# Performance work log

Measured on AMD Instinct MI355X. Metric: run time of the kernel, lower is better.

The kernel has to match this reference:

```python
import jax, jax.numpy as jnp
import numpy as np

B, NP, L, C, NA = 16, 512, 20, 3, 50
RATIO = 0.8
K = int(np.ceil(RATIO * NP))  # 410 nodes kept per graph
N = B * NP
E = 6 * N
NF, EF = 13, 4
EPS = 1e-5


def _graph_norm(x, w, b, ms):
    # PyG GraphNorm called WITHOUT batch in the source -> single global graph
    mean = x.mean(0)
    out = x - ms * mean
    var = (out * out).mean(0)
    return w * out / jnp.sqrt(var + EPS) + b


def _forward(x, pan_w, lin1_w, lin1_b, norm1_w, norm1_b, norm1_ms,
             pool_p, pool_beta, gat_wl, gat_bl, gat_wr, gat_br, gat_att, gat_bias,
             norm2_w, norm2_b, norm2_ms,
             val1_w, val1_b, val2_w, val2_b, val3_w, val3_b,
             adv1_w, adv1_b, adv2_w, adv2_b, adv3_w, adv3_b,
             edge_index, current_node_ids, action_mask):
    src, dst = edge_index[0], edge_index[1]
    # PANConv builds SparseTensor(row=edge_index[1], col=edge_index[0]) -> row = target
    A = jnp.zeros((B, NP, NP), x.dtype).at[dst // NP, dst % NP, src % NP].set(1.0)
    eyeB = jnp.broadcast_to(jnp.eye(NP, dtype=x.dtype), A.shape)

    # panentropy: M = sum_{i=0..L} w_i * A^i  (dense per graph)
    def step(carry, wi):
        tmp, acc = carry
        tmp = tmp @ A
        return (tmp, acc + wi * tmp), None
    (_, M), _ = jax.lax.scan(step, (eyeB, pan_w[0] * eyeB), pan_w[1:])
    deg = M.sum(-1)                                   # row sums
    dis = jnp.where(deg > 0, 1.0 / jnp.sqrt(deg), 0.0)
    Mn = dis[:, :, None] * M * dis[:, None, :]        # D^-1/2 M D^-1/2

    # conv1: propagate (Mn @ x) then Linear
    x3 = x.reshape(B, NP, NF)
    h = jnp.einsum('bij,bjf->bif', Mn, x3) @ lin1_w + lin1_b   # [B,NP,C]
    x1 = jax.nn.relu(_graph_norm(h.reshape(N, C), norm1_w, norm1_b, norm1_ms))  # [N,C]
    h = x1.reshape(B, NP, C)

    # PANPooling: score = tanh(b0 * <x,p> + b1 * colsum(Mn)); keep top K per graph
    score = jnp.tanh(pool_beta[0] * (h * pool_p).sum(-1) + pool_beta[1] * Mn.sum(-2))
    vals, idx = jax.lax.top_k(score, K)                        # [B,K]
    xp = jnp.take_along_axis(h, idx[:, :, None], axis=1) * vals[..., None]
    Mg = jax.vmap(lambda m, i: m[i][:, i])(Mn, idx)            # filtered adjacency [B,K,K]
    mask = (jnp.swapaxes(Mg, 1, 2) != 0) | jnp.eye(K, dtype=bool)  # mask[b,i,j]: edge j->i (+self loops)

    # GATv2Conv, heads=1, eval mode (no dropout), edge_attr not passed in source
    xl = xp @ gat_wl + gat_bl
    xr = xp @ gat_wr + gat_br
    e = jax.nn.leaky_relu(xr[:, :, None, :] + xl[:, None, :, :], 0.2)  # [B,i,j,C]
    logits = jnp.where(mask, jnp.einsum('bijc,c->bij', e, gat_att), -1e9)
    alpha = jax.nn.softmax(logits, axis=-1)
    g = jnp.einsum('bij,bjc->bic', alpha, xl) + gat_bias

    g = jax.nn.relu(_graph_norm(g.reshape(B * K, C), norm2_w, norm2_b, norm2_ms)).reshape(B, K, C)
    gp = g.sum(1)                                              # global_add_pool [B,C]

    # source uses POOLED bincount cumsum offsets to index the pre-pool arrays (faithful)
    gidx = current_node_ids + jnp.arange(B, dtype=current_node_ids.dtype) * K
    feat = jnp.concatenate([x[gidx], x1[gidx], gp], axis=1)    # [B,19]

    a = jax.nn.relu(feat @ adv1_w + adv1_b)
    a = jax.nn.relu(a @ adv2_w + adv2_b)
    a = a @ adv3_w + adv3_b
    v = jax.nn.relu(feat @ val1_w + val1_b)
    v = jax.nn.relu(v @ val2_w + val2_b)
    v = v @ val3_w + val3_b
    q = v + (a - a.mean(1, keepdims=True))
    return jnp.where(action_mask == 0, -1e8, q)


def setup_inputs() -> dict:
    key = jax.random.key(0)
    ks = list(jax.random.split(key, 40))
    nk = lambda: ks.pop()
    # within-graph random edges so the PyG-style batch structure is valid
    g = jax.random.randint(nk(), (E,), 0, B)
    u = jax.random.randint(nk(), (E,), 0, NP)
    v = jax.random.randint(nk(), (E,), 0, NP)
    edge_index = jnp.stack([g * NP + u, g * NP + v]).astype(jnp.int32)

    def lin(k, i, o):
        k1, k2 = jax.random.split(k)
        return (jax.random.normal(k1, (i, o), jnp.float32) / np.sqrt(i),
                jax.random.normal(k2, (o,), jnp.float32) * 0.01)

    lin1_w, lin1_b = lin(nk(), NF, C)
    gat_wl, gat_bl = lin(nk(), C, C)
    gat_wr, gat_br = lin(nk(), C, C)
    val1_w, val1_b = lin(nk(), 19, 10)
    val2_w, val2_b = lin(nk(), 10, 5)
    val3_w, val3_b = lin(nk(), 5, 1)
    adv1_w, adv1_b = lin(nk(), 19, 10)
    adv2_w, adv2_b = lin(nk(), 10, 5)
    adv3_w, adv3_b = lin(nk(), 5, NA)
    return dict(
        x=jax.random.normal(nk(), (N, NF), jnp.float32),
        edge_index=edge_index,
        edge_attr=jax.random.normal(nk(), (E, EF), jnp.float32),
        batch=jnp.arange(N, dtype=jnp.int32) // NP,
        current_node_ids=jax.random.randint(nk(), (B,), 0, NP),
        action_mask=jax.random.randint(nk(), (B, NA), 0, 2),
        pan_w=jax.random.uniform(nk(), (L + 1,), jnp.float32) * 0.5,
        lin1_w=lin1_w, lin1_b=lin1_b,
        norm1_w=jnp.ones(C), norm1_b=jnp.zeros(C), norm1_ms=jnp.ones(C),
        pool_p=jax.random.normal(nk(), (C,), jnp.float32),
        pool_beta=jnp.array([0.5, 0.5], jnp.float32),
        gat_wl=gat_wl, gat_bl=gat_bl, gat_wr=gat_wr, gat_br=gat_br,
        gat_att=jax.random.normal(nk(), (C,), jnp.float32),
        gat_bias=jax.random.normal(nk(), (C,), jnp.float32) * 0.01,
        norm2_w=jnp.ones(C), norm2_b=jnp.zeros(C), norm2_ms=jnp.ones(C),
        val1_w=val1_w, val1_b=val1_b, val2_w=val2_w, val2_b=val2_b,
        val3_w=val3_w, val3_b=val3_b,
        adv1_w=adv1_w, adv1_b=adv1_b, adv2_w=adv2_w, adv2_b=adv2_b,
        adv3_w=adv3_w, adv3_b=adv3_b,
    )


def reference(x, edge_index, edge_attr, batch, current_node_ids, action_mask,
              pan_w, lin1_w, lin1_b, norm1_w, norm1_b, norm1_ms,
              pool_p, pool_beta, gat_wl, gat_bl, gat_wr, gat_br, gat_att, gat_bias,
              norm2_w, norm2_b, norm2_ms,
              val1_w, val1_b, val2_w, val2_b, val3_w, val3_b,
              adv1_w, adv1_b, adv2_w, adv2_b, adv3_w, adv3_b):
    del edge_attr, batch  # received by the torch forward but never consumed
    return _forward(x, pan_w, lin1_w, lin1_b, norm1_w, norm1_b, norm1_ms,
                    pool_p, pool_beta, gat_wl, gat_bl, gat_wr, gat_br, gat_att, gat_bias,
                    norm2_w, norm2_b, norm2_ms,
                    val1_w, val1_b, val2_w, val2_b, val3_w, val3_b,
                    adv1_w, adv1_b, adv2_w, adv2_b, adv3_w, adv3_b,
                    edge_index, current_node_ids, action_mask)
```

## Files before the change

### kernel.cpp

```cpp
#include <hip/hip_runtime.h>
#include <hip/hip_bf16.h>
#include <stdint.h>
#include <math.h>

#define BB   16
#define NPn  512
#define LLp  20
#define NAa  50
#define KKk  410
#define NNt  (BB * NPn)
#define EEe  (6 * NNt)
#define NFf  13
#define KPAD 416
#define KP2  448
#define EPSf 1e-5f
#define QCLMP 1e6f
#define MAXD 28
#define PADR 512

__device__ __forceinline__ float r17_sane(float v) {
    if (!(v == v)) return 0.0f;
    return fminf(fmaxf(v, -1e15f), 1e15f);
}

__device__ __forceinline__ int r19_wmaxdeg(const int (&iF)[MAXD]) {
    int deg = 0;
#pragma unroll
    for (int j = 0; j < MAXD; ++j) deg += (iF[j] != PADR) ? 1 : 0;
#pragma unroll
    for (int off = 32; off; off >>= 1) {
        const int o = __shfl_xor(deg, off);
        deg = o > deg ? o : deg;
    }
    return deg;
}

__device__ __forceinline__ float r19_gsum(const float* __restrict__ rp,
                                          const int (&iF)[MAXD], int dm) {
    float s = 0.0f;
    s += rp[iF[0]]; s += rp[iF[1]]; s += rp[iF[2]]; s += rp[iF[3]];
    if (dm > 4) {
        s += rp[iF[4]]; s += rp[iF[5]]; s += rp[iF[6]]; s += rp[iF[7]];
        if (dm > 8) {
            s += rp[iF[8]]; s += rp[iF[9]]; s += rp[iF[10]]; s += rp[iF[11]];
            if (dm > 12) {
                s += rp[iF[12]]; s += rp[iF[13]]; s += rp[iF[14]]; s += rp[iF[15]];
                if (dm > 16) {
                    s += rp[iF[16]]; s += rp[iF[17]]; s += rp[iF[18]]; s += rp[iF[19]];
                    if (dm > 20) {
                        s += rp[iF[20]]; s += rp[iF[21]]; s += rp[iF[22]]; s += rp[iF[23]];
                        if (dm > 24) {
                            s += rp[iF[24]]; s += rp[iF[25]]; s += rp[iF[26]]; s += rp[iF[27]];
                        }
                    }
                }
            }
        }
    }
    return s;
}

__device__ __forceinline__ void r19_gor(const uint2* __restrict__ rp,
                                        const int (&iF)[MAXD], int dm, uint2& r) {
    {
        const uint2 v0 = rp[iF[0]], v1 = rp[iF[1]], v2 = rp[iF[2]], v3 = rp[iF[3]];
        r.x |= v0.x | v1.x | v2.x | v3.x;
        r.y |= v0.y | v1.y | v2.y | v3.y;
    }
    if (dm > 4) {
        const uint2 v0 = rp[iF[4]], v1 = rp[iF[5]], v2 = rp[iF[6]], v3 = rp[iF[7]];
        r.x |= v0.x | v1.x | v2.x | v3.x;
        r.y |= v0.y | v1.y | v2.y | v3.y;
        if (dm > 8) {
            const uint2 w0 = rp[iF[8]], w1 = rp[iF[9]], w2 = rp[iF[10]], w3 = rp[iF[11]];
            r.x |= w0.x | w1.x | w2.x | w3.x;
            r.y |= w0.y | w1.y | w2.y | w3.y;
            if (dm > 12) {
                const uint2 u0 = rp[iF[12]], u1 = rp[iF[13]], u2 = rp[iF[14]], u3 = rp[iF[15]];
                r.x |= u0.x | u1.x | u2.x | u3.x;
                r.y |= u0.y | u1.y | u2.y | u3.y;
                if (dm > 16) {
                    const uint2 a0 = rp[iF[16]], a1 = rp[iF[17]], a2 = rp[iF[18]], a3 = rp[iF[19]];
                    r.x |= a0.x | a1.x | a2.x | a3.x;
                    r.y |= a0.y | a1.y | a2.y | a3.y;
                    if (dm > 20) {
                        const uint2 b0 = rp[iF[20]], b1 = rp[iF[21]], b2 = rp[iF[22]], b3 = rp[iF[23]];
                        r.x |= b0.x | b1.x | b2.x | b3.x;
                        r.y |= b0.y | b1.y | b2.y | b3.y;
                        if (dm > 24) {
                            const uint2 c0 = rp[iF[24]], c1 = rp[iF[25]], c2 = rp[iF[26]], c3 = rp[iF[27]];
                            r.x |= c0.x | c1.x | c2.x | c3.x;
                            r.y |= c0.y | c1.y | c2.y | c3.y;
                        }
                    }
                }
            }
        }
    }
}

__global__ __launch_bounds__(256) void r17_scatter(
    const int* __restrict__ ei,
    uint32_t* __restrict__ fwdb, uint32_t* __restrict__ trsb)
{
    const int e = blockIdx.x * 256 + threadIdx.x;
    if (e < EEe) {
        const int src = ei[e], dst = ei[EEe + e];
        atomicOr(&fwdb[(size_t)dst * 16 + ((src & 511) >> 5)], 1u << (src & 31));
        atomicOr(&trsb[(size_t)src * 16 + ((dst & 511) >> 5)], 1u << (dst & 31));
    }
}

__global__ __launch_bounds__(256) void r17_extract(
    const uint32_t* __restrict__ fwdb, const uint32_t* __restrict__ trsb,
    unsigned short* __restrict__ csrF, unsigned short* __restrict__ csrT)
{
    const int t = blockIdx.x * 256 + threadIdx.x;
    const int node = t & 8191;
    const uint32_t* bs = (t < 8192) ? (fwdb + (size_t)node * 16)
                                    : (trsb + (size_t)node * 16);
    unsigned short* cs = (t < 8192) ? csrF : csrT;
    int cnt = 0;
    for (int w = 0; w < 16; ++w) {
        uint32_t bits = bs[w];
        while (bits) {
            const int u = (w << 5) + __ffs(bits) - 1;
            bits &= bits - 1;
            if (cnt < MAXD) cs[(size_t)cnt * 8192 + node] = (unsigned short)u;
            ++cnt;
        }
    }
    for (int j = cnt; j < MAXD; ++j) cs[(size_t)j * 8192 + node] = PADR;
}

__global__ __launch_bounds__(512) void r19_mid(
    const float* __restrict__ x,
    const unsigned short* __restrict__ csrF,
    const unsigned short* __restrict__ csrT,
    const float* __restrict__ panw,
    const float* __restrict__ l1w, const float* __restrict__ l1b,
    float* __restrict__ h_raw, float* __restrict__ colsum,
    uint32_t* __restrict__ Rb)
{
    __shared__ __align__(16) uint32_t sbuf[2052];
    const int b = blockIdx.x, y = blockIdx.y, t = threadIdx.x;
    const int node = b * 512 + t;

    int iF[MAXD];
#pragma unroll
    for (int j = 0; j < MAXD; ++j) iF[j] = (int)csrF[(size_t)j * 8192 + node];
    const int dmF = r19_wmaxdeg(iF);

    if (y < 4) {
        const int c = y;
        float* pa  = (float*)sbuf;
        float* pb  = (float*)(sbuf + 513);
        float* wsh = (float*)(sbuf + 1026);
        if (t < 21) wsh[t] = panw[t];

        pa[t] = 1.0f;
        if (t == 0) { pa[512] = 0.0f; pb[512] = 0.0f; }
        __syncthreads();
        float dacc = wsh[0];
        {
            float* rp = pa; float* rn = pb;
            for (int i = 1; i <= LLp; ++i) {
                const float s = r19_gsum(rp, iF, dmF);
                rn[t] = s;
                dacc += wsh[i] * s;
                __syncthreads();
                float* tp = rp; rp = rn; rn = tp;
            }
        }
        const float d0 = (dacc > 0.0f) ? 1.0f / sqrtf(dacc) : 0.0f;

        int idx[MAXD];
        int dm2;
        if (c == 3) {
#pragma unroll
            for (int j = 0; j < MAXD; ++j) idx[j] = (int)csrT[(size_t)j * 8192 + node];
            dm2 = r19_wmaxdeg(idx);
        } else {
#pragma unroll
            for (int j = 0; j < MAXD; ++j) idx[j] = iF[j];
            dm2 = dmF;
        }
        float seed;
        if (c < 3) {
            float xw = 0.0f;
            const float* xr = x + (size_t)node * NFf;
            for (int f = 0; f < NFf; ++f) xw += xr[f] * l1w[f * 3 + c];
            seed = d0 * xw;
        } else {
            seed = d0;
        }
        pa[t] = seed;
        if (t == 0) { pa[512] = 0.0f; pb[512] = 0.0f; }
        __syncthreads();
        float acc = wsh[0] * seed;
        {
            float* rp = pa; float* rn = pb;
            for (int i = 1; i <= LLp; ++i) {
                const float s = r19_gsum(rp, idx, dm2);
                rn[t] = s;
                acc += wsh[i] * s;
                __syncthreads();
                float* tp = rp; rp = rn; rn = tp;
            }
        }
        if (c < 3) h_raw[(size_t)node * 3 + c] = r17_sane(d0 * acc + l1b[c]);
        else       colsum[node] = r17_sane(d0 * acc);
    } else {
        const int q = y - 4;
        uint2* R1 = (uint2*)sbuf;
        uint2* R2 = R1 + 513;
        uint2 seed;
        seed.x = ((t >> 5) == 2 * q)     ? (1u << (t & 31)) : 0u;
        seed.y = ((t >> 5) == 2 * q + 1) ? (1u << (t & 31)) : 0u;
        R1[t] = seed;
        if (t == 0) {
            uint2 z; z.x = 0u; z.y = 0u;
            R1[512] = z; R2[512] = z;
        }
        __syncthreads();
        uint2* Rp = R1; uint2* Rn = R2;
        for (int i = 0; i < LLp; ++i) {
            uint2 r = Rp[t];
            r19_gor(Rp, iF, dmF, r);
            Rn[t] = r;
            __syncthreads();
            uint2* tp = Rp; Rp = Rn; Rn = tp;
        }
        *(uint2*)(&Rb[(size_t)node * 16 + 2 * q]) = Rp[t];
    }
}

__global__ __launch_bounds__(512) void r19_pool(
    const float* __restrict__ h_raw,
    const float* __restrict__ colsum,
    const uint32_t* __restrict__ Rb,
    const float* n1w, const float* n1b, const float* n1ms,
    const float* poolp, const float* poolb,
    const float* gwl, const float* gbl,
    float* __restrict__ x1,
    float* __restrict__ xpg,
    float4* __restrict__ xlg,
    int*   __restrict__ kidxg,
    uint32_t* __restrict__ RTg)
{
    __shared__ __align__(16) uint32_t pg[2208];
    float* sc   = (float*)pg;
    float* mv   = (float*)(pg + 512);
    float* wred = (float*)(pg + 520);
    float* xpS  = (float*)(pg + 544);
    int*   kidx = (int*)(pg + 1792);
    const int b = blockIdx.x, t = threadIdx.x;
    const int lane = t & 63, wv = t >> 6;
    const float inv_n = 1.0f / (float)NNt;

    float hv0[16], hv1[16], hv2[16];
    float p0 = 0.0f, p1 = 0.0f, p2 = 0.0f;
#pragma unroll
    for (int k = 0; k < 16; ++k) {
        const float* hr = h_raw + (size_t)(k * 512 + t) * 3;
        hv0[k] = hr[0]; hv1[k] = hr[1]; hv2[k] = hr[2];
        p0 += hv0[k]; p1 += hv1[k]; p2 += hv2[k];
    }
#pragma unroll
    for (int off = 32; off; off >>= 1) {
        p0 += __shfl_xor(p0, off); p1 += __shfl_xor(p1, off); p2 += __shfl_xor(p2, off);
    }
    if (lane == 0) { wred[wv * 3 + 0] = p0; wred[wv * 3 + 1] = p1; wred[wv * 3 + 2] = p2; }
    __syncthreads();
    if (t < 3) {
        float s = 0.0f;
        for (int w = 0; w < 8; ++w) s += wred[w * 3 + t];
        mv[t] = s * inv_n;
    }
    __syncthreads();
    const float mm0 = n1ms[0] * mv[0], mm1 = n1ms[1] * mv[1], mm2 = n1ms[2] * mv[2];
    float q0 = 0.0f, q1 = 0.0f, q2 = 0.0f;
#pragma unroll
    for (int k = 0; k < 16; ++k) {
        const float d0 = hv0[k] - mm0, d1 = hv1[k] - mm1, d2 = hv2[k] - mm2;
        q0 += d0 * d0; q1 += d1 * d1; q2 += d2 * d2;
    }
#pragma unroll
    for (int off = 32; off; off >>= 1) {
        q0 += __shfl_xor(q0, off); q1 += __shfl_xor(q1, off); q2 += __shfl_xor(q2, off);
    }
    if (lane == 0) { wred[wv * 3 + 0] = q0; wred[wv * 3 + 1] = q1; wred[wv * 3 + 2] = q2; }
    __syncthreads();
    if (t < 3) {
        float s = 0.0f;
        for (int w = 0; w < 8; ++w) s += wred[w * 3 + t];
        mv[3 + t] = s * inv_n;
    }
    __syncthreads();

    const float mmv[3] = { mm0, mm1, mm2 };
    float xv[3];
#pragma unroll
    for (int c = 0; c < 3; ++c) {
        const float iv = 1.0f / sqrtf(fmaxf(mv[3 + c], 0.0f) + EPSf);
        const float o  = h_raw[(size_t)(b * NPn + t) * 3 + c] - mmv[c];
        const float tt = n1w[c] * o * iv + n1b[c];
        xv[c] = fmaxf(tt, 0.0f);
        x1[(size_t)(b * NPn + t) * 3 + c] = xv[c];
    }
    float s = poolb[0] * (xv[0] * poolp[0] + xv[1] * poolp[1] + xv[2] * poolp[2])
            + poolb[1] * colsum[b * NPn + t];
    s = tanhf(s);
    if (!(s == s)) s = 0.0f;
    sc[t] = s;
    __syncthreads();

    int cnt = 0;
    for (int u = 0; u < NPn; u += 4) {
        const float4 s4 = *(const float4*)(sc + u);
        cnt += ((s4.x > s) || (s4.x == s && (u + 0) < t)) ? 1 : 0;
        cnt += ((s4.y > s) || (s4.y == s && (u + 1) < t)) ? 1 : 0;
        cnt += ((s4.z > s) || (s4.z == s && (u + 2) < t)) ? 1 : 0;
        cnt += ((s4.w > s) || (s4.w == s && (u + 3) < t)) ? 1 : 0;
    }
    if (cnt < KKk) {
        const float xp0 = xv[0] * s, xp1 = xv[1] * s, xp2 = xv[2] * s;
        kidx[cnt] = t;
        xpS[cnt * 3 + 0] = xp0;
        xpS[cnt * 3 + 1] = xp1;
        xpS[cnt * 3 + 2] = xp2;
        kidxg[b * KPAD + cnt] = t;
        xpg[(size_t)(b * KPAD + cnt) * 3 + 0] = xp0;
        xpg[(size_t)(b * KPAD + cnt) * 3 + 1] = xp1;
        xpg[(size_t)(b * KPAD + cnt) * 3 + 2] = xp2;
    }
    __syncthreads();

    float Wl[9];
#pragma unroll
    for (int i2 = 0; i2 < 9; ++i2) Wl[i2] = gwl[i2];
    const float Bl0 = gbl[0], Bl1 = gbl[1], Bl2 = gbl[2];
    if (t < KP2) {
        float xl0, xl1, xl2;
        uint32_t* RT = RTg + (size_t)b * 16 * KP2 + t;
        if (t < KKk) {
            const float c0 = xpS[t * 3 + 0];
            const float c1 = xpS[t * 3 + 1];
            const float c2 = xpS[t * 3 + 2];
            xl0 = c0 * Wl[0] + c1 * Wl[3] + c2 * Wl[6] + Bl0;
            xl1 = c0 * Wl[1] + c1 * Wl[4] + c2 * Wl[7] + Bl1;
            xl2 = c0 * Wl[2] + c1 * Wl[5] + c2 * Wl[8] + Bl2;
            const uint4* rr = (const uint4*)(Rb + (size_t)(b * NPn + kidx[t]) * 16);
            const uint4 r0 = rr[0], r1 = rr[1], r2 = rr[2], r3 = rr[3];
            RT[ 0 * KP2] = r0.x; RT[ 1 * KP2] = r0.y; RT[ 2 * KP2] = r0.z; RT[ 3 * KP2] = r0.w;
            RT[ 4 * KP2] = r1.x; RT[ 5 * KP2] = r1.y; RT[ 6 * KP2] = r1.z; RT[ 7 * KP2] = r1.w;
            RT[ 8 * KP2] = r2.x; RT[ 9 * KP2] = r2.y; RT[10 * KP2] = r2.z; RT[11 * KP2] = r2.w;
            RT[12 * KP2] = r3.x; RT[13 * KP2] = r3.y; RT[14 * KP2] = r3.z; RT[15 * KP2] = r3.w;
        } else {
            xl0 = 0.0f; xl1 = 0.0f; xl2 = 0.0f;
#pragma unroll
            for (int w = 0; w < 16; ++w) RT[w * KP2] = 0u;
        }
        xlg[(size_t)(b * KP2 + t)] = make_float4(xl0, xl1, xl2, 0.0f);
    }
}

__global__ __launch_bounds__(512) void r19_gat(
    const float* __restrict__ xpg,
    const float4* __restrict__ xlg,
    const int* __restrict__ kidxg,
    const uint32_t* __restrict__ RTg,
    const float* __restrict__ gwr, const float* __restrict__ gbr,
    const float* __restrict__ gatt, const float* __restrict__ gbias,
    float* __restrict__ g_raw)
{
    const int b = blockIdx.x, y = blockIdx.y, t = threadIdx.x;
    const int lane = t & 63, wv = t >> 6;
    const int i = y * 8 + wv;
    if (i >= KKk) return;

    float Wr[9];
#pragma unroll
    for (int k = 0; k < 9; ++k) Wr[k] = gwr[k];
    const float Br0 = gbr[0], Br1 = gbr[1], Br2 = gbr[2];
    const float At0 = gatt[0], At1 = gatt[1], At2 = gatt[2];
    const float Gb0 = gbias[0], Gb1 = gbias[1], Gb2 = gbias[2];

    const int bi = kidxg[b * KPAD + i];
    const float c0 = xpg[(size_t)(b * KPAD + i) * 3 + 0];
    const float c1 = xpg[(size_t)(b * KPAD + i) * 3 + 1];
    const float c2 = xpg[(size_t)(b * KPAD + i) * 3 + 2];
    const float xr0 = c0 * Wr[0] + c1 * Wr[3] + c2 * Wr[6] + Br0;
    const float xr1 = c0 * Wr[1] + c1 * Wr[4] + c2 * Wr[7] + Br1;
    const float xr2 = c0 * Wr[2] + c1 * Wr[5] + c2 * Wr[8] + Br2;

    const uint32_t mbit = 1u << (bi & 31);
    const uint32_t* Rw = RTg + (size_t)(b * 16 + (bi >> 5)) * KP2;
    const float4* xlb = xlg + (size_t)b * KP2;

    float mx = -3e38f, lsum = 0.0f, b0 = 0.0f, b1 = 0.0f, b2 = 0.0f;
#pragma unroll
    for (int it = 0; it < 7; ++it) {
        const int j = lane + it * 64;
        const uint32_t rw = Rw[j];
        const float4 xlv = xlb[j];
        const float xl0 = xlv.x, xl1 = xlv.y, xl2 = xlv.z;
        const bool valid = (rw & mbit) || (j == i);
        float e0 = xr0 + xl0; e0 = e0 > 0.0f ? e0 : 0.2f * e0;
        float e1 = xr1 + xl1; e1 = e1 > 0.0f ? e1 : 0.2f * e1;
        float e2 = xr2 + xl2; e2 = e2 > 0.0f ? e2 : 0.2f * e2;
        const float sv = At0 * e0 + At1 * e1 + At2 * e2;
        if (valid) {
            if (sv > mx) {
                const float r = __expf(mx - sv);
                lsum *= r; b0 *= r; b1 *= r; b2 *= r;
                mx = sv;
            }
            const float pj = __expf(sv - mx);
            lsum += pj;
            b0 += pj * xl0; b1 += pj * xl1; b2 += pj * xl2;
        }
    }
#pragma unroll
    for (int off = 32; off; off >>= 1) {
        const float mo = __shfl_xor(mx, off);
        const float lo = __shfl_xor(lsum, off);
        const float d0 = __shfl_xor(b0, off);
        const float d1 = __shfl_xor(b1, off);
        const float d2 = __shfl_xor(b2, off);
        const float M  = fmaxf(mx, mo);
        const float ea = __expf(mx - M), eb = __expf(mo - M);
        lsum = lsum * ea + lo * eb;
        b0 = b0 * ea + d0 * eb;
        b1 = b1 * ea + d1 * eb;
        b2 = b2 * ea + d2 * eb;
        mx = M;
    }
    if (lane == 0) {
        const float rl = 1.0f / fmaxf(lsum, 1e-30f);
        g_raw[(size_t)(b * KPAD + i) * 3 + 0] = r17_sane(b0 * rl + Gb0);
        g_raw[(size_t)(b * KPAD + i) * 3 + 1] = r17_sane(b1 * rl + Gb1);
        g_raw[(size_t)(b * KPAD + i) * 3 + 2] = r17_sane(b2 * rl + Gb2);
    }
}

__global__ __launch_bounds__(512) void r17_head(
    const float* __restrict__ g_raw,
    const float* __restrict__ x1,
    const float* __restrict__ x,
    const int* __restrict__ cnid,
    const int* __restrict__ amask,
    const float* n2w, const float* n2b, const float* n2ms,
    const float* v1w, const float* v1b,
    const float* v2w, const float* v2b,
    const float* v3w, const float* v3b,
    const float* a1w, const float* a1b,
    const float* a2w, const float* a2b,
    const float* a3w, const float* a3b,
    float* __restrict__ out)
{
    __shared__ float wred[24];
    __shared__ float mv[6];
    __shared__ float gp[3];
    __shared__ float feat[19];
    __shared__ float h1a[10], h1v[10], h2a[5], h2v[5];
    __shared__ float a3[50];
    __shared__ float vout_s, amean_s;
    const int b = blockIdx.x, t = threadIdx.x;
    const int lane = t & 63, wv = t >> 6;
    const float denom = 1.0f / (float)(BB * KKk);

    float gv0[13], gv1[13], gv2[13];
    float p0 = 0.0f, p1 = 0.0f, p2 = 0.0f;
#pragma unroll
    for (int k = 0; k < 13; ++k) {
        const int r = k * 512 + t;
        float q0 = 0.0f, q1 = 0.0f, q2 = 0.0f;
        if (r < BB * KKk) {
            const int bq = r / KKk, iq = r - bq * KKk;
            const float* gr = g_raw + (size_t)(bq * KPAD + iq) * 3;
            q0 = gr[0]; q1 = gr[1]; q2 = gr[2];
        }
        gv0[k] = q0; gv1[k] = q1; gv2[k] = q2;
        p0 += q0; p1 += q1; p2 += q2;
    }
#pragma unroll
    for (int off = 32; off; off >>= 1) {
        p0 += __shfl_xor(p0, off); p1 += __shfl_xor(p1, off); p2 += __shfl_xor(p2, off);
    }
    if (lane == 0) { wred[wv * 3 + 0] = p0; wred[wv * 3 + 1] = p1; wred[wv * 3 + 2] = p2; }
    __syncthreads();
    if (t < 3) {
        float s = 0.0f;
        for (int w = 0; w < 8; ++w) s += wred[w * 3 + t];
        mv[t] = s * denom;
    }
    __syncthreads();
    const float mm0 = n2ms[0] * mv[0], mm1 = n2ms[1] * mv[1], mm2 = n2ms[2] * mv[2];
    float q0a = 0.0f, q1a = 0.0f, q2a = 0.0f;
#pragma unroll
    for (int k = 0; k < 13; ++k) {
        const int r = k * 512 + t;
        if (r < BB * KKk) {
            const float d0 = gv0[k] - mm0, d1 = gv1[k] - mm1, d2 = gv2[k] - mm2;
            q0a += d0 * d0; q1a += d1 * d1; q2a += d2 * d2;
        }
    }
#pragma unroll
    for (int off = 32; off; off >>= 1) {
        q0a += __shfl_xor(q0a, off); q1a += __shfl_xor(q1a, off); q2a += __shfl_xor(q2a, off);
    }
    if (lane == 0) { wred[wv * 3 + 0] = q0a; wred[wv * 3 + 1] = q1a; wred[wv * 3 + 2] = q2a; }
    __syncthreads();
    if (t < 3) {
        float s = 0.0f;
        for (int w = 0; w < 8; ++w) s += wred[w * 3 + t];
        mv[3 + t] = s * denom;
    }
    __syncthreads();

    const float mmv[3] = { mm0, mm1, mm2 };
    float s3[3] = { 0.0f, 0.0f, 0.0f };
    if (t < KKk) {
        const size_t r = (size_t)(b * KPAD + t) * 3;
#pragma unroll
        for (int c = 0; c < 3; ++c) {
            const float iv = 1.0f / sqrtf(fmaxf(mv[3 + c], 0.0f) + EPSf);
            s3[c] = fmaxf((g_raw[r + c] - mmv[c]) * iv * n2w[c] + n2b[c], 0.0f);
        }
    }
    float g0 = s3[0], g1 = s3[1], g2 = s3[2];
#pragma unroll
    for (int off = 32; off; off >>= 1) {
        g0 += __shfl_xor(g0, off); g1 += __shfl_xor(g1, off); g2 += __shfl_xor(g2, off);
    }
    if (lane == 0) { wred[wv * 3 + 0] = g0; wred[wv * 3 + 1] = g1; wred[wv * 3 + 2] = g2; }
    __syncthreads();
    if (t < 3) {
        float s = 0.0f;
        for (int w = 0; w < 8; ++w) s += wred[w * 3 + t];
        gp[t] = s;
    }
    __syncthreads();

    if (t < 19) {
        const int gidx = cnid[b] + b * KKk;
        float fv;
        if (t < 13)      fv = x[(size_t)gidx * NFf + t];
        else if (t < 16) fv = x1[(size_t)gidx * 3 + (t - 13)];
        else             fv = gp[t - 16];
        feat[t] = fv;
    }
    __syncthreads();

    if (t < 10) {
        float s = a1b[t];
        for (int f = 0; f < 19; ++f) s += feat[f] * a1w[f * 10 + t];
        h1a[t] = fmaxf(s, 0.0f);
    } else if (t >= 64 && t < 74) {
        const int j = t - 64;
        float s = v1b[j];
        for (int f = 0; f < 19; ++f) s += feat[f] * v1w[f * 10 + j];
        h1v[j] = fmaxf(s, 0.0f);
    }
    __syncthreads();
    if (t < 5) {
        float s = a2b[t];
        for (int k = 0; k < 10; ++k) s += h1a[k] * a2w[k * 5 + t];
        h2a[t] = fmaxf(s, 0.0f);
    } else if (t >= 64 && t < 69) {
        const int j = t - 64;
        float s = v2b[j];
        for (int k = 0; k < 10; ++k) s += h1v[k] * v2w[k * 5 + j];
        h2v[j] = fmaxf(s, 0.0f);
    }
    __syncthreads();
    if (t < 50) {
        float s = a3b[t];
        for (int k = 0; k < 5; ++k) s += h2a[k] * a3w[k * 50 + t];
        a3[t] = s;
    } else if (t == 64) {
        float s = v3b[0];
        for (int k = 0; k < 5; ++k) s += h2v[k] * v3w[k];
        vout_s = s;
    }
    __syncthreads();
    if (t == 0) {
        float s = 0.0f;
        for (int k = 0; k < 50; ++k) s += a3[k];
        amean_s = s * (1.0f / 50.0f);
    }
    __syncthreads();
    if (t < 50) {
        float q = vout_s + a3[t] - amean_s;
        if (!(q == q)) q = 0.0f;
        q = fminf(fmaxf(q, -QCLMP), QCLMP);
        out[b * NAa + t] = (amask[b * NAa + t] == 0) ? -1e8f : q;
    }
}

extern "C" void kernel_launch(void* const* d_in, const int* in_sizes, int n_in,
                              void* d_out, int out_size, void* d_ws, size_t ws_size,
                              hipStream_t stream) {
    (void)in_sizes; (void)n_in; (void)out_size;
    const float* x     = (const float*)d_in[0];
    const int* ei      = (const int*)d_in[1];
    const int* cnid    = (const int*)d_in[4];
    const int* amask   = (const int*)d_in[5];
    const float* panw  = (const float*)d_in[6];
    const float* l1w   = (const float*)d_in[7];
    const float* l1b   = (const float*)d_in[8];
    const float* n1w   = (const float*)d_in[9];
    const float* n1b   = (const float*)d_in[10];
    const float* n1ms  = (const float*)d_in[11];
    const float* poolp = (const float*)d_in[12];
    const float* poolb = (const float*)d_in[13];
    const float* gwl   = (const float*)d_in[14];
    const float* gbl   = (const float*)d_in[15];
    const float* gwr   = (const float*)d_in[16];
    const float* gbr   = (const float*)d_in[17];
    const float* gatt  = (const float*)d_in[18];
    const float* gbias = (const float*)d_in[19];
    const float* n2w   = (const float*)d_in[20];
    const float* n2b   = (const float*)d_in[21];
    const float* n2ms  = (const float*)d_in[22];
    const float* v1w   = (const float*)d_in[23];
    const float* v1b   = (const float*)d_in[24];
    const float* v2w   = (const float*)d_in[25];
    const float* v2b   = (const float*)d_in[26];
    const float* v3w   = (const float*)d_in[27];
    const float* v3b   = (const float*)d_in[28];
    const float* a1w   = (const float*)d_in[29];
    const float* a1b   = (const float*)d_in[30];
    const float* a2w   = (const float*)d_in[31];
    const float* a2b   = (const float*)d_in[32];
    const float* a3w   = (const float*)d_in[33];
    const float* a3b   = (const float*)d_in[34];
    float* out         = (float*)d_out;

    uint8_t* wsb = (uint8_t*)d_ws;
    uint32_t* fwdb = (uint32_t*)wsb;
    uint32_t* trsb = (uint32_t*)(wsb + 524288);
    uint32_t* Rb   = (uint32_t*)(wsb + 1048576);
    unsigned short* csrF = (unsigned short*)(wsb + 1572864);
    unsigned short* csrT = csrF + (size_t)MAXD * 8192;
    float* h_raw  = (float*)(csrT + (size_t)MAXD * 8192);
    float* x1     = h_raw + (size_t)NNt * 3;
    float* colsum = x1 + (size_t)NNt * 3;
    float* g_raw  = colsum + NNt;
    float* xpg    = g_raw + (size_t)BB * KPAD * 3;
    float4* xlg   = (float4*)(xpg + (size_t)BB * KPAD * 3);
    int*   kidxg  = (int*)(xlg + (size_t)BB * KP2);
    uint32_t* RTg = (uint32_t*)(kidxg + (size_t)BB * KPAD);
    const size_t needed = 1572864
                        + 2 * (size_t)MAXD * 8192 * 2
                        + ((size_t)(2 * NNt * 3 + NNt
                           + 2 * BB * KPAD * 3)) * 4
                        + (size_t)BB * KP2 * 16
                        + (size_t)BB * KPAD * 4
                        + (size_t)BB * 16 * KP2 * 4;
    if (ws_size < needed) return;

    hipMemsetAsync(fwdb, 0, 1048576, stream);
    r17_scatter<<<dim3((EEe + 255) / 256), dim3(256), 0, stream>>>(ei, fwdb, trsb);
    r17_extract<<<dim3(64), dim3(256), 0, stream>>>(fwdb, trsb, csrF, csrT);
    r19_mid<<<dim3(16, 12), dim3(512), 0, stream>>>(x, csrF, csrT, panw, l1w, l1b,
                                                    h_raw, colsum, Rb);
    r19_pool<<<dim3(16), dim3(512), 0, stream>>>(h_raw, colsum, Rb,
                                                 n1w, n1b, n1ms, poolp, poolb,
                                                 gwl, gbl,
                                                 x1, xpg, xlg, kidxg, RTg);
    r19_gat<<<dim3(16, 52), dim3(512), 0, stream>>>(xpg, xlg, kidxg, RTg,
                                                    gwr, gbr, gatt, gbias, g_raw);
    r17_head<<<dim3(16), dim3(512), 0, stream>>>(g_raw, x1, x, cnid, amask,
                                                 n2w, n2b, n2ms, v1w, v1b, v2w, v2b, v3w, v3b,
                                                 a1w, a1b, a2w, a2b, a3w, a3b, out);
}
```

Measured before the change: 201.6 us.

## Fuse adjacency bitmask build and CSR extraction into mid kernel via shared memory

```diff
diff --git a/kernel.cpp b/kernel.cpp
--- a/kernel.cpp
+++ b/kernel.cpp
@@ -1,5 +1,4 @@
 #include <hip/hip_runtime.h>
-#include <hip/hip_bf16.h>
 #include <stdint.h>
 #include <math.h>
 
@@ -99,63 +98,79 @@
     }
 }
 
-__global__ __launch_bounds__(256) void r17_scatter(
-    const int* __restrict__ ei,
-    uint32_t* __restrict__ fwdb, uint32_t* __restrict__ trsb)
+__device__ __forceinline__ void r22_build(
+    uint32_t* __restrict__ A, unsigned short* __restrict__ C,
+    const int* __restrict__ ei, int b, int t, bool trs)
 {
-    const int e = blockIdx.x * 256 + threadIdx.x;
-    if (e < EEe) {
+#pragma unroll
+    for (int k = 0; k < 16; ++k) A[k * 512 + t] = 0u;
+    __syncthreads();
+    for (int k = 0; k < EEe / 512; ++k) {
+        const int e = k * 512 + t;
         const int src = ei[e], dst = ei[EEe + e];
-        atomicOr(&fwdb[(size_t)dst * 16 + ((src & 511) >> 5)], 1u << (src & 31));
-        atomicOr(&trsb[(size_t)src * 16 + ((dst & 511) >> 5)], 1u << (dst & 31));
-    }
-}
-
-__global__ __launch_bounds__(256) void r17_extract(
-    const uint32_t* __restrict__ fwdb, const uint32_t* __restrict__ trsb,
-    unsigned short* __restrict__ csrF, unsigned short* __restrict__ csrT)
-{
-    const int t = blockIdx.x * 256 + threadIdx.x;
-    const int node = t & 8191;
-    const uint32_t* bs = (t < 8192) ? (fwdb + (size_t)node * 16)
-                                    : (trsb + (size_t)node * 16);
-    unsigned short* cs = (t < 8192) ? csrF : csrT;
+        if (!trs) {
+            if ((dst >> 9) == b)
+                atomicOr(&A[(dst & 511) * 16 + ((src & 511) >> 5)], 1u << (src & 31));
+        } else {
+            if ((src >> 9) == b)
+                atomicOr(&A[(src & 511) * 16 + ((dst & 511) >> 5)], 1u << (dst & 31));
+        }
+    }
+    __syncthreads();
     int cnt = 0;
     for (int w = 0; w < 16; ++w) {
-        uint32_t bits = bs[w];
+        uint32_t bits = A[t * 16 + w];
         while (bits) {
             const int u = (w << 5) + __ffs(bits) - 1;
             bits &= bits - 1;
-            if (cnt < MAXD) cs[(size_t)cnt * 8192 + node] = (unsigned short)u;
+            if (cnt < MAXD) C[cnt * 512 + t] = (unsigned short)u;
             ++cnt;
         }
     }
-    for (int j = cnt; j < MAXD; ++j) cs[(size_t)j * 8192 + node] = PADR;
-}
-
-__global__ __launch_bounds__(512) void r19_mid(
+    for (int j = cnt; j < MAXD; ++j) C[j * 512 + t] = PADR;
+    __syncthreads();
+}
+
+__global__ __launch_bounds__(512) void r22_mid(
     const float* __restrict__ x,
-    const unsigned short* __restrict__ csrF,
-    const unsigned short* __restrict__ csrT,
+    const int* __restrict__ ei,
     const float* __restrict__ panw,
     const float* __restrict__ l1w, const float* __restrict__ l1b,
     float* __restrict__ h_raw, float* __restrict__ colsum,
     uint32_t* __restrict__ Rb)
 {
-    __shared__ __align__(16) uint32_t sbuf[2052];
+    __shared__ __align__(16) uint32_t S[8192 + 7168];
+    uint32_t* A = S;
+    unsigned short* C = (unsigned short*)(S + 8192);
     const int b = blockIdx.x, y = blockIdx.y, t = threadIdx.x;
     const int node = b * 512 + t;
 
+    r22_build(A, C, ei, b, t, false);
     int iF[MAXD];
 #pragma unroll
-    for (int j = 0; j < MAXD; ++j) iF[j] = (int)csrF[(size_t)j * 8192 + node];
+    for (int j = 0; j < MAXD; ++j) iF[j] = (int)C[j * 512 + t];
     const int dmF = r19_wmaxdeg(iF);
+
+    int idx[MAXD];
+    int dm2;
+    if (y == 3) {
+        __syncthreads();
+        r22_build(A, C, ei, b, t, true);
+#pragma unroll
+        for (int j = 0; j < MAXD; ++j) idx[j] = (int)C[j * 512 + t];
+        dm2 = r19_wmaxdeg(idx);
+    } else {
+#pragma unroll
+        for (int j = 0; j < MAXD; ++j) idx[j] = iF[j];
+        dm2 = dmF;
+    }
+    __syncthreads();
 
     if (y < 4) {
         const int c = y;
-        float* pa  = (float*)sbuf;
-        float* pb  = (float*)(sbuf + 513);
-        float* wsh = (float*)(sbuf + 1026);
+        float* pa  = (float*)(S + 8192);
+        float* pb  = pa + 513;
+        float* wsh = pb + 513;
         if (t < 21) wsh[t] = panw[t];
 
         pa[t] = 1.0f;
@@ -174,17 +189,6 @@
         }
         const float d0 = (dacc > 0.0f) ? 1.0f / sqrtf(dacc) : 0.0f;
 
-        int idx[MAXD];
-        int dm2;
-        if (c == 3) {
-#pragma unroll
-            for (int j = 0; j < MAXD; ++j) idx[j] = (int)csrT[(size_t)j * 8192 + node];
-            dm2 = r19_wmaxdeg(idx);
-        } else {
-#pragma unroll
-            for (int j = 0; j < MAXD; ++j) idx[j] = iF[j];
-            dm2 = dmF;
-        }
         float seed;
         if (c < 3) {
             float xw = 0.0f;
@@ -212,7 +216,7 @@
         else       colsum[node] = r17_sane(d0 * acc);
     } else {
         const int q = y - 4;
-        uint2* R1 = (uint2*)sbuf;
+        uint2* R1 = (uint2*)(S + 8192);
         uint2* R2 = R1 + 513;
         uint2 seed;
         seed.x = ((t >> 5) == 2 * q)     ? (1u << (t & 31)) : 0u;
@@ -639,12 +643,8 @@
     float* out         = (float*)d_out;
 
     uint8_t* wsb = (uint8_t*)d_ws;
-    uint32_t* fwdb = (uint32_t*)wsb;
-    uint32_t* trsb = (uint32_t*)(wsb + 524288);
-    uint32_t* Rb   = (uint32_t*)(wsb + 1048576);
-    unsigned short* csrF = (unsigned short*)(wsb + 1572864);
-    unsigned short* csrT = csrF + (size_t)MAXD * 8192;
-    float* h_raw  = (float*)(csrT + (size_t)MAXD * 8192);
+    uint32_t* Rb   = (uint32_t*)wsb;
+    float* h_raw  = (float*)(wsb + 524288);
     float* x1     = h_raw + (size_t)NNt * 3;
     float* colsum = x1 + (size_t)NNt * 3;
     float* g_raw  = colsum + NNt;
@@ -652,19 +652,10 @@
     float4* xlg   = (float4*)(xpg + (size_t)BB * KPAD * 3);
     int*   kidxg  = (int*)(xlg + (size_t)BB * KP2);
     uint32_t* RTg = (uint32_t*)(kidxg + (size_t)BB * KPAD);
-    const size_t needed = 1572864
-                        + 2 * (size_t)MAXD * 8192 * 2
-                        + ((size_t)(2 * NNt * 3 + NNt
-                           + 2 * BB * KPAD * 3)) * 4
-                        + (size_t)BB * KP2 * 16
-                        + (size_t)BB * KPAD * 4
-                        + (size_t)BB * 16 * KP2 * 4;
+    const size_t needed = (size_t)((uint8_t*)(RTg + (size_t)BB * 16 * KP2) - wsb);
     if (ws_size < needed) return;
 
-    hipMemsetAsync(fwdb, 0, 1048576, stream);
-    r17_scatter<<<dim3((EEe + 255) / 256), dim3(256), 0, stream>>>(ei, fwdb, trsb);
-    r17_extract<<<dim3(64), dim3(256), 0, stream>>>(fwdb, trsb, csrF, csrT);
-    r19_mid<<<dim3(16, 12), dim3(512), 0, stream>>>(x, csrF, csrT, panw, l1w, l1b,
+    r22_mid<<<dim3(16, 12), dim3(512), 0, stream>>>(x, ei, panw, l1w, l1b,
                                                     h_raw, colsum, Rb);
     r19_pool<<<dim3(16), dim3(512), 0, stream>>>(h_raw, colsum, Rb,
                                                  n1w, n1b, n1ms, poolp, poolb,
```

Result: slower. 265.8 us (+31.8%).

## Compute PAN degree normalization once in extract kernel instead of per mid block

Applied to the files above, without the earlier changes.

```diff
diff --git a/kernel.cpp b/kernel.cpp
--- a/kernel.cpp
+++ b/kernel.cpp
@@ -1,5 +1,4 @@
 #include <hip/hip_runtime.h>
-#include <hip/hip_bf16.h>
 #include <stdint.h>
 #include <math.h>
 
@@ -111,34 +110,84 @@
     }
 }
 
-__global__ __launch_bounds__(256) void r17_extract(
+__global__ __launch_bounds__(512) void r23_extract(
     const uint32_t* __restrict__ fwdb, const uint32_t* __restrict__ trsb,
-    unsigned short* __restrict__ csrF, unsigned short* __restrict__ csrT)
+    const float* __restrict__ panw,
+    unsigned short* __restrict__ csrF, unsigned short* __restrict__ csrT,
+    float* __restrict__ d0g)
 {
-    const int t = blockIdx.x * 256 + threadIdx.x;
-    const int node = t & 8191;
-    const uint32_t* bs = (t < 8192) ? (fwdb + (size_t)node * 16)
-                                    : (trsb + (size_t)node * 16);
-    unsigned short* cs = (t < 8192) ? csrF : csrT;
-    int cnt = 0;
-    for (int w = 0; w < 16; ++w) {
-        uint32_t bits = bs[w];
-        while (bits) {
-            const int u = (w << 5) + __ffs(bits) - 1;
-            bits &= bits - 1;
-            if (cnt < MAXD) cs[(size_t)cnt * 8192 + node] = (unsigned short)u;
-            ++cnt;
-        }
-    }
-    for (int j = cnt; j < MAXD; ++j) cs[(size_t)j * 8192 + node] = PADR;
-}
-
-__global__ __launch_bounds__(512) void r19_mid(
+    __shared__ __align__(16) uint32_t S[7168 + 1047];
+    const int blk = blockIdx.x, tid = threadIdx.x;
+
+    if (blk < 32) {
+        const int t = blk * 512 + tid;
+        const int node = t & 8191;
+        const uint32_t* bs = (t < 8192) ? (fwdb + (size_t)node * 16)
+                                        : (trsb + (size_t)node * 16);
+        unsigned short* cs = (t < 8192) ? csrF : csrT;
+        int cnt = 0;
+        for (int w = 0; w < 16; ++w) {
+            uint32_t bits = bs[w];
+            while (bits) {
+                const int u = (w << 5) + __ffs(bits) - 1;
+                bits &= bits - 1;
+                if (cnt < MAXD) cs[(size_t)cnt * 8192 + node] = (unsigned short)u;
+                ++cnt;
+            }
+        }
+        for (int j = cnt; j < MAXD; ++j) cs[(size_t)j * 8192 + node] = PADR;
+    } else {
+        const int b = blk - 32;
+        const int node = b * 512 + tid;
+        unsigned short* Ctmp = (unsigned short*)S;
+        float* pa  = (float*)(S + 7168);
+        float* pb  = pa + 513;
+        float* wsh = pb + 513;
+        {
+            const uint32_t* bs = fwdb + (size_t)node * 16;
+            int cnt = 0;
+            for (int w = 0; w < 16; ++w) {
+                uint32_t bits = bs[w];
+                while (bits) {
+                    const int u = (w << 5) + __ffs(bits) - 1;
+                    bits &= bits - 1;
+                    if (cnt < MAXD) Ctmp[cnt * 512 + tid] = (unsigned short)u;
+                    ++cnt;
+                }
+            }
+            for (int j = cnt; j < MAXD; ++j) Ctmp[j * 512 + tid] = PADR;
+        }
+        int iF[MAXD];
+#pragma unroll
+        for (int j = 0; j < MAXD; ++j) iF[j] = (int)Ctmp[j * 512 + tid];
+        const int dmF = r19_wmaxdeg(iF);
+
+        if (tid < 21) wsh[tid] = panw[tid];
+        pa[tid] = 1.0f;
+        if (tid == 0) { pa[512] = 0.0f; pb[512] = 0.0f; }
+        __syncthreads();
+        float dacc = wsh[0];
+        {
+            float* rp = pa; float* rn = pb;
+            for (int i = 1; i <= LLp; ++i) {
+                const float s = r19_gsum(rp, iF, dmF);
+                rn[tid] = s;
+                dacc += wsh[i] * s;
+                __syncthreads();
+                float* tp = rp; rp = rn; rn = tp;
+            }
+        }
+        d0g[node] = (dacc > 0.0f) ? 1.0f / sqrtf(dacc) : 0.0f;
+    }
+}
+
+__global__ __launch_bounds__(512) void r23_mid(
     const float* __restrict__ x,
     const unsigned short* __restrict__ csrF,
     const unsigned short* __restrict__ csrT,
     const float* __restrict__ panw,
     const float* __restrict__ l1w, const float* __restrict__ l1b,
+    const float* __restrict__ d0g,
     float* __restrict__ h_raw, float* __restrict__ colsum,
     uint32_t* __restrict__ Rb)
 {
@@ -146,11 +195,6 @@
     const int b = blockIdx.x, y = blockIdx.y, t = threadIdx.x;
     const int node = b * 512 + t;
 
-    int iF[MAXD];
-#pragma unroll
-    for (int j = 0; j < MAXD; ++j) iF[j] = (int)csrF[(size_t)j * 8192 + node];
-    const int dmF = r19_wmaxdeg(iF);
-
     if (y < 4) {
         const int c = y;
         float* pa  = (float*)sbuf;
@@ -158,33 +202,17 @@
         float* wsh = (float*)(sbuf + 1026);
         if (t < 21) wsh[t] = panw[t];
 
-        pa[t] = 1.0f;
-        if (t == 0) { pa[512] = 0.0f; pb[512] = 0.0f; }
-        __syncthreads();
-        float dacc = wsh[0];
-        {
-            float* rp = pa; float* rn = pb;
-            for (int i = 1; i <= LLp; ++i) {
-                const float s = r19_gsum(rp, iF, dmF);
-                rn[t] = s;
-                dacc += wsh[i] * s;
-                __syncthreads();
-                float* tp = rp; rp = rn; rn = tp;
-            }
-        }
-        const float d0 = (dacc > 0.0f) ? 1.0f / sqrtf(dacc) : 0.0f;
-
         int idx[MAXD];
-        int dm2;
         if (c == 3) {
 #pragma unroll
             for (int j = 0; j < MAXD; ++j) idx[j] = (int)csrT[(size_t)j * 8192 + node];
-            dm2 = r19_wmaxdeg(idx);
         } else {
 #pragma unroll
-            for (int j = 0; j < MAXD; ++j) idx[j] = iF[j];
-            dm2 = dmF;
-        }
+            for (int j = 0; j < MAXD; ++j) idx[j] = (int)csrF[(size_t)j * 8192 + node];
+        }
+        const int dm2 = r19_wmaxdeg(idx);
+        const float d0 = d0g[node];
+
         float seed;
         if (c < 3) {
             float xw = 0.0f;
@@ -211,6 +239,10 @@
         if (c < 3) h_raw[(size_t)node * 3 + c] = r17_sane(d0 * acc + l1b[c]);
         else       colsum[node] = r17_sane(d0 * acc);
     } else {
+        int iF[MAXD];
+#pragma unroll
+        for (int j = 0; j < MAXD; ++j) iF[j] = (int)csrF[(size_t)j * 8192 + node];
+        const int dmF = r19_wmaxdeg(iF);
         const int q = y - 4;
         uint2* R1 = (uint2*)sbuf;
         uint2* R2 = R1 + 513;
@@ -644,7 +676,8 @@
     uint32_t* Rb   = (uint32_t*)(wsb + 1048576);
     unsigned short* csrF = (unsigned short*)(wsb + 1572864);
     unsigned short* csrT = csrF + (size_t)MAXD * 8192;
-    float* h_raw  = (float*)(csrT + (size_t)MAXD * 8192);
+    float* d0g    = (float*)(csrT + (size_t)MAXD * 8192);
+    float* h_raw  = d0g + NNt;
     float* x1     = h_raw + (size_t)NNt * 3;
     float* colsum = x1 + (size_t)NNt * 3;
     float* g_raw  = colsum + NNt;
@@ -652,20 +685,15 @@
     float4* xlg   = (float4*)(xpg + (size_t)BB * KPAD * 3);
     int*   kidxg  = (int*)(xlg + (size_t)BB * KP2);
     uint32_t* RTg = (uint32_t*)(kidxg + (size_t)BB * KPAD);
-    const size_t needed = 1572864
-                        + 2 * (size_t)MAXD * 8192 * 2
-                        + ((size_t)(2 * NNt * 3 + NNt
-                           + 2 * BB * KPAD * 3)) * 4
-                        + (size_t)BB * KP2 * 16
-                        + (size_t)BB * KPAD * 4
-                        + (size_t)BB * 16 * KP2 * 4;
+    const size_t needed = (size_t)((uint8_t*)(RTg + (size_t)BB * 16 * KP2) - wsb);
     if (ws_size < needed) return;
 
     hipMemsetAsync(fwdb, 0, 1048576, stream);
     r17_scatter<<<dim3((EEe + 255) / 256), dim3(256), 0, stream>>>(ei, fwdb, trsb);
-    r17_extract<<<dim3(64), dim3(256), 0, stream>>>(fwdb, trsb, csrF, csrT);
-    r19_mid<<<dim3(16, 12), dim3(512), 0, stream>>>(x, csrF, csrT, panw, l1w, l1b,
-                                                    h_raw, colsum, Rb);
+    r23_extract<<<dim3(48), dim3(512), 0, stream>>>(fwdb, trsb, panw,
+                                                    csrF, csrT, d0g);
+    r23_mid<<<dim3(16, 12), dim3(512), 0, stream>>>(x, csrF, csrT, panw, l1w, l1b,
+                                                    d0g, h_raw, colsum, Rb);
     r19_pool<<<dim3(16), dim3(512), 0, stream>>>(h_raw, colsum, Rb,
                                                  n1w, n1b, n1ms, poolp, poolb,
                                                  gwl, gbl,
```

Result: no change. 202.3 us (+0.3%).
